# Kernel tuning notes

Measured on AMD Instinct MI355X. Metric: run time of the kernel, lower is better.

## Reference

```python
import jax, jax.numpy as jnp
import numpy as np

HIDDEN = 1024
SENT = 1024
NS = 8192
NK = 8192


def setup_inputs() -> dict:
    key = jax.random.key(0)
    ks = jax.random.split(key, 6)
    scale = 0.02
    return {
        "sentences_embedding": jax.random.normal(ks[0], (NS, SENT), dtype=jnp.float32),
        "knowledge_embedding": jax.random.normal(ks[1], (NK, 2 * HIDDEN), dtype=jnp.float32),
        "Ws": jax.random.normal(ks[2], (HIDDEN, SENT), dtype=jnp.float32) * scale,
        "bs": jnp.zeros((HIDDEN,), dtype=jnp.float32),
        "Wk": jax.random.normal(ks[3], (HIDDEN, 2 * HIDDEN), dtype=jnp.float32) * scale,
        "bk": jnp.zeros((HIDDEN,), dtype=jnp.float32),
    }


def reference(sentences_embedding, knowledge_embedding, Ws, bs, Wk, bk):
    # S: [Ns, hidden], K: [Nk, hidden] (torch Linear: x @ W.T + b)
    S = sentences_embedding @ Ws.T + bs
    K = knowledge_embedding @ Wk.T + bk
    V = knowledge_embedding  # [Nk, 2*hidden]
    scores = S @ K.T  # [Ns, Nk]
    # NOTE: softmax over dim=0 (across sentences), per the original module
    attns = jax.nn.softmax(scores, axis=0)
    fused_knowledge = attns @ V  # [Ns, 2*hidden]
    return (attns, fused_knowledge)
```

## Files before the change

### kernel.cpp

```cpp
#include <hip/hip_runtime.h>
#include <hip/hip_bf16.h>
#include <math.h>

typedef __bf16 bf16_t;
typedef __bf16 bf16x8 __attribute__((ext_vector_type(8)));
typedef __bf16 bf16x4v __attribute__((ext_vector_type(4)));
typedef float floatx4 __attribute__((ext_vector_type(4)));

#define BM 128
#define BN 128
#define BK 64
#define LDT 72

__device__ __forceinline__ void gload_lds16(const void* g, void* l) {
    __builtin_amdgcn_global_load_lds(
        (__attribute__((address_space(1))) void*)g,
        (__attribute__((address_space(3))) void*)l,
        16, 0, 0);
}

__device__ __forceinline__ void split8(const float* p, bf16x8& hi, bf16x8& lo) {
    const float4* q = (const float4*)p;
    float4 a = q[0], b = q[1];
    float v[8] = { a.x, a.y, a.z, a.w, b.x, b.y, b.z, b.w };
#pragma unroll
    for (int i = 0; i < 8; ++i) {
        bf16_t h = (bf16_t)v[i];
        hi[i] = h;
        lo[i] = (bf16_t)(v[i] - (float)h);
    }
}

__device__ __forceinline__ bf16x8 ld8cvt(const float* p) {
    const float4* q = (const float4*)p;
    float4 a = q[0], b = q[1];
    bf16x8 r;
    r[0] = (bf16_t)a.x; r[1] = (bf16_t)a.y; r[2] = (bf16_t)a.z; r[3] = (bf16_t)a.w;
    r[4] = (bf16_t)b.x; r[5] = (bf16_t)b.y; r[6] = (bf16_t)b.z; r[7] = (bf16_t)b.w;
    return r;
}

template<bool OUT_SPLIT, bool HAS_BIAS>
__global__ __launch_bounds__(256, 2)
void gemm_nt_split(const float* __restrict__ A, const float* __restrict__ B,
                   const float* __restrict__ bias,
                   void* __restrict__ C0, bf16_t* __restrict__ Clo,
                   int M, int N, int K)
{
    __shared__ bf16_t Ah[BM * LDT];
    __shared__ bf16_t Al[BM * LDT];
    __shared__ bf16_t Bh[BN * LDT];
    __shared__ bf16_t Bl[BN * LDT];

    const int t    = threadIdx.x;
    const int m0   = blockIdx.x * BM;
    const int n0   = blockIdx.y * BN;
    const int lane = t & 63;
    const int wm   = ((t >> 6) & 1) * 64;
    const int wn   = (t >> 7) * 64;
    const int lr   = lane & 15;
    const int lg   = lane >> 4;

    floatx4 acc[4][4] = {};

    for (int k0 = 0; k0 < K; k0 += BK) {
#pragma unroll
        for (int i = 0; i < 4; ++i) {
            int idx = t + i * 256;
            int row = idx >> 3;
            int col = (idx & 7) << 3;
            bf16x8 h, l;
            split8(&A[(size_t)(m0 + row) * K + k0 + col], h, l);
            *(bf16x8*)&Ah[row * LDT + col] = h;
            *(bf16x8*)&Al[row * LDT + col] = l;
            split8(&B[(size_t)(n0 + row) * K + k0 + col], h, l);
            *(bf16x8*)&Bh[row * LDT + col] = h;
            *(bf16x8*)&Bl[row * LDT + col] = l;
        }
        __syncthreads();
#pragma unroll
        for (int ks = 0; ks < BK; ks += 32) {
            bf16x8 ah[4], al[4], bh[4], bl[4];
#pragma unroll
            for (int mi = 0; mi < 4; ++mi) {
                ah[mi] = *(const bf16x8*)&Ah[(wm + mi * 16 + lr) * LDT + ks + lg * 8];
                al[mi] = *(const bf16x8*)&Al[(wm + mi * 16 + lr) * LDT + ks + lg * 8];
            }
#pragma unroll
            for (int ni = 0; ni < 4; ++ni) {
                bh[ni] = *(const bf16x8*)&Bh[(wn + ni * 16 + lr) * LDT + ks + lg * 8];
                bl[ni] = *(const bf16x8*)&Bl[(wn + ni * 16 + lr) * LDT + ks + lg * 8];
            }
#pragma unroll
            for (int mi = 0; mi < 4; ++mi)
#pragma unroll
                for (int ni = 0; ni < 4; ++ni) {
                    acc[mi][ni] = __builtin_amdgcn_mfma_f32_16x16x32_bf16(ah[mi], bh[ni], acc[mi][ni], 0, 0, 0);
                    acc[mi][ni] = __builtin_amdgcn_mfma_f32_16x16x32_bf16(ah[mi], bl[ni], acc[mi][ni], 0, 0, 0);
                    acc[mi][ni] = __builtin_amdgcn_mfma_f32_16x16x32_bf16(al[mi], bh[ni], acc[mi][ni], 0, 0, 0);
                }
        }
        __syncthreads();
    }

#pragma unroll
    for (int mi = 0; mi < 4; ++mi)
#pragma unroll
        for (int ni = 0; ni < 4; ++ni) {
            int col = n0 + wn + ni * 16 + lr;
            float bv = 0.0f;
            if constexpr (HAS_BIAS) bv = bias[col];
#pragma unroll
            for (int r = 0; r < 4; ++r) {
                int row = m0 + wm + mi * 16 + lg * 4 + r;
                float v = acc[mi][ni][r] + bv;
                if constexpr (OUT_SPLIT) {
                    bf16_t h = (bf16_t)v;
                    ((bf16_t*)C0)[(size_t)row * N + col] = h;
                    Clo[(size_t)row * N + col] = (bf16_t)(v - (float)h);
                } else {
                    ((float*)C0)[(size_t)row * N + col] = v;
                }
            }
        }
}

__global__ __launch_bounds__(256, 2)
void gemm_nt_pre_async(const bf16_t* __restrict__ Ahi, const bf16_t* __restrict__ Alo,
                       const bf16_t* __restrict__ Bhi, const bf16_t* __restrict__ Blo,
                       float* __restrict__ C, float* __restrict__ pm,
                       float* __restrict__ pz, int M, int N, int K)
{
    __shared__ bf16_t Ah[BM * BK];
    __shared__ bf16_t Al[BM * BK];
    __shared__ bf16_t Bh[BN * BK];
    __shared__ bf16_t Bl[BN * BK];
    __shared__ float red_m[2][128];
    __shared__ float red_z[2][128];

    const int t    = threadIdx.x;
    const int m0   = blockIdx.x * BM;
    const int n0   = blockIdx.y * BN;
    const int lane = t & 63;
    const int wv   = t >> 6;
    const int widm = (t >> 6) & 1;
    const int wm   = widm * 64;
    const int wn   = (t >> 7) * 64;
    const int lr   = lane & 15;
    const int lg   = lane >> 4;
    const int lrow = lane >> 3;
    const int lcol = (((lane & 7) ^ lrow) * 8);
    const int swz  = (lr & 7) << 3;

    floatx4 acc[4][4] = {};

    for (int k0 = 0; k0 < K; k0 += BK) {
#pragma unroll
        for (int i = 0; i < 4; ++i) {
            const int seg = wv * 4 + i;
            const int row = seg * 8 + lrow;
            const size_t ga = (size_t)(m0 + row) * K + k0 + lcol;
            const size_t gb = (size_t)(n0 + row) * K + k0 + lcol;
            gload_lds16(&Ahi[ga], &Ah[seg * 512]);
            gload_lds16(&Alo[ga], &Al[seg * 512]);
            gload_lds16(&Bhi[gb], &Bh[seg * 512]);
            gload_lds16(&Blo[gb], &Bl[seg * 512]);
        }
        __syncthreads();
#pragma unroll
        for (int ks = 0; ks < BK; ks += 32) {
            const int cA = (ks + lg * 8) ^ swz;
            bf16x8 ah[4], al[4], bh[4], bl[4];
#pragma unroll
            for (int mi = 0; mi < 4; ++mi) {
                ah[mi] = *(const bf16x8*)&Ah[(wm + mi * 16 + lr) * BK + cA];
                al[mi] = *(const bf16x8*)&Al[(wm + mi * 16 + lr) * BK + cA];
            }
#pragma unroll
            for (int ni = 0; ni < 4; ++ni) {
                bh[ni] = *(const bf16x8*)&Bh[(wn + ni * 16 + lr) * BK + cA];
                bl[ni] = *(const bf16x8*)&Bl[(wn + ni * 16 + lr) * BK + cA];
            }
#pragma unroll
            for (int mi = 0; mi < 4; ++mi)
#pragma unroll
                for (int ni = 0; ni < 4; ++ni) {
                    acc[mi][ni] = __builtin_amdgcn_mfma_f32_16x16x32_bf16(ah[mi], bh[ni], acc[mi][ni], 0, 0, 0);
                    acc[mi][ni] = __builtin_amdgcn_mfma_f32_16x16x32_bf16(ah[mi], bl[ni], acc[mi][ni], 0, 0, 0);
                    acc[mi][ni] = __builtin_amdgcn_mfma_f32_16x16x32_bf16(al[mi], bh[ni], acc[mi][ni], 0, 0, 0);
                }
        }
        __syncthreads();
    }

#pragma unroll
    for (int mi = 0; mi < 4; ++mi)
#pragma unroll
        for (int ni = 0; ni < 4; ++ni) {
            int col = n0 + wn + ni * 16 + lr;
#pragma unroll
            for (int r = 0; r < 4; ++r) {
                int row = m0 + wm + mi * 16 + lg * 4 + r;
                C[(size_t)row * N + col] = acc[mi][ni][r];
            }
        }

#pragma unroll
    for (int ni = 0; ni < 4; ++ni) {
        float lm = -INFINITY;
#pragma unroll
        for (int mi = 0; mi < 4; ++mi)
#pragma unroll
            for (int r = 0; r < 4; ++r) lm = fmaxf(lm, acc[mi][ni][r]);
        float lz = 0.0f;
#pragma unroll
        for (int mi = 0; mi < 4; ++mi)
#pragma unroll
            for (int r = 0; r < 4; ++r) lz += __expf(acc[mi][ni][r] - lm);
#pragma unroll
        for (int off = 16; off <= 32; off <<= 1) {
            float om = __shfl_xor(lm, off);
            float oz = __shfl_xor(lz, off);
            float nm = fmaxf(lm, om);
            lz = lz * __expf(lm - nm) + oz * __expf(om - nm);
            lm = nm;
        }
        if (lg == 0) {
            red_m[widm][wn + ni * 16 + lr] = lm;
            red_z[widm][wn + ni * 16 + lr] = lz;
        }
    }
    __syncthreads();
    if (t < 128) {
        float a = red_m[0][t], b = red_m[1][t];
        float za = red_z[0][t], zb = red_z[1][t];
        float mb = fmaxf(a, b);
        float z  = za * __expf(a - mb) + zb * __expf(b - mb);
        pm[(size_t)blockIdx.x * 8192 + n0 + t] = mb;
        pz[(size_t)blockIdx.x * 8192 + n0 + t] = z;
    }
}

__global__ __launch_bounds__(256, 2)
void gemm_nt_bf16_async(const bf16_t* __restrict__ A, const bf16_t* __restrict__ B,
                        float* __restrict__ C, int M, int N, int K)
{
    __shared__ bf16_t As[BM * BK];
    __shared__ bf16_t Bs[BN * BK];

    const int t    = threadIdx.x;
    const int m0   = blockIdx.x * BM;
    const int n0   = blockIdx.y * BN;
    const int lane = t & 63;
    const int wv   = t >> 6;
    const int wm   = ((t >> 6) & 1) * 64;
    const int wn   = (t >> 7) * 64;
    const int lr   = lane & 15;
    const int lg   = lane >> 4;
    const int lrow = lane >> 3;
    const int lcol = (((lane & 7) ^ lrow) * 8);
    const int swz  = (lr & 7) << 3;

    floatx4 acc[4][4] = {};

    for (int k0 = 0; k0 < K; k0 += BK) {
#pragma unroll
        for (int i = 0; i < 4; ++i) {
            const int seg = wv * 4 + i;
            const int row = seg * 8 + lrow;
            gload_lds16(&A[(size_t)(m0 + row) * K + k0 + lcol], &As[seg * 512]);
            gload_lds16(&B[(size_t)(n0 + row) * K + k0 + lcol], &Bs[seg * 512]);
        }
        __syncthreads();
#pragma unroll
        for (int ks = 0; ks < BK; ks += 32) {
            const int cA = (ks + lg * 8) ^ swz;
            bf16x8 a[4], b[4];
#pragma unroll
            for (int mi = 0; mi < 4; ++mi)
                a[mi] = *(const bf16x8*)&As[(wm + mi * 16 + lr) * BK + cA];
#pragma unroll
            for (int ni = 0; ni < 4; ++ni)
                b[ni] = *(const bf16x8*)&Bs[(wn + ni * 16 + lr) * BK + cA];
#pragma unroll
            for (int mi = 0; mi < 4; ++mi)
#pragma unroll
                for (int ni = 0; ni < 4; ++ni)
                    acc[mi][ni] = __builtin_amdgcn_mfma_f32_16x16x32_bf16(
                        a[mi], b[ni], acc[mi][ni], 0, 0, 0);
        }
        __syncthreads();
    }

#pragma unroll
    for (int mi = 0; mi < 4; ++mi)
#pragma unroll
        for (int ni = 0; ni < 4; ++ni) {
            int col = n0 + wn + ni * 16 + lr;
#pragma unroll
            for (int r = 0; r < 4; ++r) {
                int row = m0 + wm + mi * 16 + lg * 4 + r;
                C[(size_t)row * N + col] = acc[mi][ni][r];
            }
        }
}

__global__ __launch_bounds__(256)
void transpose_to_bf16(const float* __restrict__ src, bf16_t* __restrict__ dst,
                       int R, int Ccols)
{
    __shared__ float tile[64][65];
    const int r0 = blockIdx.x * 64;
    const int c0 = blockIdx.y * 64;
    const int tr = threadIdx.x >> 4;
    const int tc = (threadIdx.x & 15) * 4;
#pragma unroll
    for (int i = 0; i < 4; ++i) {
        int r = tr + i * 16;
        float4 v = *(const float4*)&src[(size_t)(r0 + r) * Ccols + c0 + tc];
        tile[r][tc + 0] = v.x; tile[r][tc + 1] = v.y;
        tile[r][tc + 2] = v.z; tile[r][tc + 3] = v.w;
    }
    __syncthreads();
#pragma unroll
    for (int i = 0; i < 4; ++i) {
        int c = tr + i * 16;
        bf16x4v o = { (bf16_t)tile[tc + 0][c], (bf16_t)tile[tc + 1][c],
                      (bf16_t)tile[tc + 2][c], (bf16_t)tile[tc + 3][c] };
        *(bf16x4v*)&dst[(size_t)(c0 + c) * R + r0 + tc] = o;
    }
}

__global__ __launch_bounds__(256)
void col_softmax_combine64(const float* __restrict__ pm, const float* __restrict__ pz,
                           float* __restrict__ mf, float* __restrict__ iz)
{
    int j = blockIdx.x * 256 + threadIdx.x;
    float m = -INFINITY;
#pragma unroll
    for (int c = 0; c < 64; ++c) m = fmaxf(m, pm[(size_t)c * 8192 + j]);
    float z = 0.0f;
#pragma unroll
    for (int c = 0; c < 64; ++c) z += pz[(size_t)c * 8192 + j] * __expf(pm[(size_t)c * 8192 + j] - m);
    mf[j] = m;
    iz[j] = 1.0f / z;
}

__global__ __launch_bounds__(256)
void normalize_attn(float* __restrict__ sc, const float* __restrict__ mf,
                    const float* __restrict__ iz)
{
    size_t base = ((size_t)blockIdx.x * 256 + threadIdx.x) * 4;
    int j = (int)(base & 8191);
    float4 s  = *(float4*)&sc[base];
    float4 m4 = *(const float4*)&mf[j];
    float4 z4 = *(const float4*)&iz[j];
    s.x = __expf(s.x - m4.x) * z4.x;
    s.y = __expf(s.y - m4.y) * z4.y;
    s.z = __expf(s.z - m4.z) * z4.z;
    s.w = __expf(s.w - m4.w) * z4.w;
    *(float4*)&sc[base] = s;
}

__global__ __launch_bounds__(256)
void normalize_attn_bf16(float* __restrict__ sc, const float* __restrict__ mf,
                         const float* __restrict__ iz, bf16_t* __restrict__ ab)
{
    size_t base = ((size_t)blockIdx.x * 256 + threadIdx.x) * 4;
    int j = (int)(base & 8191);
    float4 s  = *(float4*)&sc[base];
    float4 m4 = *(const float4*)&mf[j];
    float4 z4 = *(const float4*)&iz[j];
    s.x = __expf(s.x - m4.x) * z4.x;
    s.y = __expf(s.y - m4.y) * z4.y;
    s.z = __expf(s.z - m4.z) * z4.z;
    s.w = __expf(s.w - m4.w) * z4.w;
    *(float4*)&sc[base] = s;
    bf16x4v b = { (bf16_t)s.x, (bf16_t)s.y, (bf16_t)s.z, (bf16_t)s.w };
    *(bf16x4v*)&ab[base] = b;
}

extern "C" void kernel_launch(void* const* d_in, const int* in_sizes, int n_in,
                              void* d_out, int out_size, void* d_ws, size_t ws_size,
                              hipStream_t stream) {
    const float* sent  = (const float*)d_in[0];
    const float* knowl = (const float*)d_in[1];
    const float* Ws    = (const float*)d_in[2];
    const float* bs    = (const float*)d_in[3];
    const float* Wk    = (const float*)d_in[4];
    const float* bk    = (const float*)d_in[5];

    float* attns = (float*)d_out;
    float* fused = (float*)d_out + (size_t)8192 * 8192;

    const size_t MB = 1024 * 1024;
    char* ws = (char*)d_ws;
    bf16_t* Shi = (bf16_t*)(ws + 0 * MB);
    bf16_t* Slo = (bf16_t*)(ws + 16 * MB);
    bf16_t* Khi = (bf16_t*)(ws + 32 * MB);
    bf16_t* Klo = (bf16_t*)(ws + 48 * MB);

    dim3 blk(256);
    gemm_nt_split<true, true><<<dim3(64, 8), blk, 0, stream>>>(
        sent, Ws, bs, Shi, Slo, 8192, 1024, 1024);
    gemm_nt_split<true, true><<<dim3(64, 8), blk, 0, stream>>>(
        knowl, Wk, bk, Khi, Klo, 8192, 1024, 2048);

    const size_t NEED = 166 * MB;
    if (ws_size >= NEED) {
        bf16_t* Ab = (bf16_t*)(ws);
        bf16_t* Vt = (bf16_t*)(ws + 128 * MB);
        float*  pm = (float*)(ws + 160 * MB);
        float*  pz = (float*)(ws + 162 * MB);
        float*  mf = (float*)(ws + 164 * MB);
        float*  iz = mf + 8192;

        transpose_to_bf16<<<dim3(128, 32), blk, 0, stream>>>(knowl, Vt, 8192, 2048);
        gemm_nt_pre_async<<<dim3(64, 64), blk, 0, stream>>>(
            Shi, Slo, Khi, Klo, attns, pm, pz, 8192, 8192, 1024);
        col_softmax_combine64<<<dim3(32), blk, 0, stream>>>(pm, pz, mf, iz);
        normalize_attn_bf16<<<dim3(65536), blk, 0, stream>>>(attns, mf, iz, Ab);
        gemm_nt_bf16_async<<<dim3(64, 16), blk, 0, stream>>>(
            Ab, Vt, fused, 8192, 2048, 8192);
    } else {
        float* pm = (float*)(ws + 64 * MB);
        float* pz = (float*)(ws + 66 * MB);
        float* mf = (float*)(ws + 68 * MB);
        float* iz = mf + 8192;

        gemm_nt_pre_async<<<dim3(64, 64), blk, 0, stream>>>(
            Shi, Slo, Khi, Klo, attns, pm, pz, 8192, 8192, 1024);
        col_softmax_combine64<<<dim3(32), blk, 0, stream>>>(pm, pz, mf, iz);
        bf16_t* Ab = (bf16_t*)(ws);
        normalize_attn_bf16<<<dim3(65536), blk, 0, stream>>>(attns, mf, iz, Ab);
        bf16_t* Vt = (bf16_t*)(ws + 128 * MB);
        transpose_to_bf16<<<dim3(128, 32), blk, 0, stream>>>(knowl, Vt, 8192, 2048);
        gemm_nt_bf16_async<<<dim3(64, 16), blk, 0, stream>>>(
            Ab, Vt, fused, 8192, 2048, 8192);
    }
}
```

Baseline: 1.286 ms.

## Pre-split fp32 projection inputs into bf16 hi/lo and use async-LDS projection GEMM

Adds a split_pair kernel that converts the sentence, knowledge and weight matrices into bf16 hi/lo pairs up front, and a new projection GEMM that streams these pre-split operands straight into LDS with global_load_lds. The split conversion is no longer redone inside each projection tile. It also reorders the fallback path and moves the V transpose after the scores GEMM. The cost is extra full passes over the inputs and a larger workspace requirement (172MB), with the old path kept as a fallback.

```diff
diff --git a/kernel.cpp b/kernel.cpp
--- a/kernel.cpp
+++ b/kernel.cpp
@@ -31,13 +31,15 @@
     }
 }
 
-__device__ __forceinline__ bf16x8 ld8cvt(const float* p) {
-    const float4* q = (const float4*)p;
-    float4 a = q[0], b = q[1];
-    bf16x8 r;
-    r[0] = (bf16_t)a.x; r[1] = (bf16_t)a.y; r[2] = (bf16_t)a.z; r[3] = (bf16_t)a.w;
-    r[4] = (bf16_t)b.x; r[5] = (bf16_t)b.y; r[6] = (bf16_t)b.z; r[7] = (bf16_t)b.w;
-    return r;
+__global__ __launch_bounds__(256)
+void split_pair(const float* __restrict__ x, bf16_t* __restrict__ hi,
+                bf16_t* __restrict__ lo)
+{
+    size_t i = ((size_t)blockIdx.x * 256 + threadIdx.x) * 8;
+    bf16x8 h, l;
+    split8(&x[i], h, l);
+    *(bf16x8*)&hi[i] = h;
+    *(bf16x8*)&lo[i] = l;
 }
 
 template<bool OUT_SPLIT, bool HAS_BIAS>
@@ -121,6 +123,89 @@
                 } else {
                     ((float*)C0)[(size_t)row * N + col] = v;
                 }
+            }
+        }
+}
+
+__global__ __launch_bounds__(256, 2)
+void gemm_nt_pre_split_out(const bf16_t* __restrict__ Ahi, const bf16_t* __restrict__ Alo,
+                           const bf16_t* __restrict__ Bhi, const bf16_t* __restrict__ Blo,
+                           const float* __restrict__ bias,
+                           bf16_t* __restrict__ Chi, bf16_t* __restrict__ Clo,
+                           int M, int N, int K)
+{
+    __shared__ bf16_t Ah[BM * BK];
+    __shared__ bf16_t Al[BM * BK];
+    __shared__ bf16_t Bh[BN * BK];
+    __shared__ bf16_t Bl[BN * BK];
+
+    const int t    = threadIdx.x;
+    const int m0   = blockIdx.x * BM;
+    const int n0   = blockIdx.y * BN;
+    const int lane = t & 63;
+    const int wv   = t >> 6;
+    const int wm   = ((t >> 6) & 1) * 64;
+    const int wn   = (t >> 7) * 64;
+    const int lr   = lane & 15;
+    const int lg   = lane >> 4;
+    const int lrow = lane >> 3;
+    const int lcol = (((lane & 7) ^ lrow) * 8);
+    const int swz  = (lr & 7) << 3;
+
+    floatx4 acc[4][4] = {};
+
+    for (int k0 = 0; k0 < K; k0 += BK) {
+#pragma unroll
+        for (int i = 0; i < 4; ++i) {
+            const int seg = wv * 4 + i;
+            const int row = seg * 8 + lrow;
+            const size_t ga = (size_t)(m0 + row) * K + k0 + lcol;
+            const size_t gb = (size_t)(n0 + row) * K + k0 + lcol;
+            gload_lds16(&Ahi[ga], &Ah[seg * 512]);
+            gload_lds16(&Alo[ga], &Al[seg * 512]);
+            gload_lds16(&Bhi[gb], &Bh[seg * 512]);
+            gload_lds16(&Blo[gb], &Bl[seg * 512]);
+        }
+        __syncthreads();
+#pragma unroll
+        for (int ks = 0; ks < BK; ks += 32) {
+            const int cA = (ks + lg * 8) ^ swz;
+            bf16x8 ah[4], al[4], bh[4], bl[4];
+#pragma unroll
+            for (int mi = 0; mi < 4; ++mi) {
+                ah[mi] = *(const bf16x8*)&Ah[(wm + mi * 16 + lr) * BK + cA];
+                al[mi] = *(const bf16x8*)&Al[(wm + mi * 16 + lr) * BK + cA];
+            }
+#pragma unroll
+            for (int ni = 0; ni < 4; ++ni) {
+                bh[ni] = *(const bf16x8*)&Bh[(wn + ni * 16 + lr) * BK + cA];
+                bl[ni] = *(const bf16x8*)&Bl[(wn + ni * 16 + lr) * BK + cA];
+            }
+#pragma unroll
+            for (int mi = 0; mi < 4; ++mi)
+#pragma unroll
+                for (int ni = 0; ni < 4; ++ni) {
+                    acc[mi][ni] = __builtin_amdgcn_mfma_f32_16x16x32_bf16(ah[mi], bh[ni], acc[mi][ni], 0, 0, 0);
+                    acc[mi][ni] = __builtin_amdgcn_mfma_f32_16x16x32_bf16(ah[mi], bl[ni], acc[mi][ni], 0, 0, 0);
+                    acc[mi][ni] = __builtin_amdgcn_mfma_f32_16x16x32_bf16(al[mi], bh[ni], acc[mi][ni], 0, 0, 0);
+                }
+        }
+        __syncthreads();
+    }
+
+#pragma unroll
+    for (int mi = 0; mi < 4; ++mi)
+#pragma unroll
+        for (int ni = 0; ni < 4; ++ni) {
+            int col = n0 + wn + ni * 16 + lr;
+            float bv = bias[col];
+#pragma unroll
+            for (int r = 0; r < 4; ++r) {
+                int row = m0 + wm + mi * 16 + lg * 4 + r;
+                float v = acc[mi][ni][r] + bv;
+                bf16_t h = (bf16_t)v;
+                Chi[(size_t)row * N + col] = h;
+                Clo[(size_t)row * N + col] = (bf16_t)(v - (float)h);
             }
         }
 }
@@ -347,22 +432,6 @@
 }
 
 __global__ __launch_bounds__(256)
-void normalize_attn(float* __restrict__ sc, const float* __restrict__ mf,
-                    const float* __restrict__ iz)
-{
-    size_t base = ((size_t)blockIdx.x * 256 + threadIdx.x) * 4;
-    int j = (int)(base & 8191);
-    float4 s  = *(float4*)&sc[base];
-    float4 m4 = *(const float4*)&mf[j];
-    float4 z4 = *(const float4*)&iz[j];
-    s.x = __expf(s.x - m4.x) * z4.x;
-    s.y = __expf(s.y - m4.y) * z4.y;
-    s.z = __expf(s.z - m4.z) * z4.z;
-    s.w = __expf(s.w - m4.w) * z4.w;
-    *(float4*)&sc[base] = s;
-}
-
-__global__ __launch_bounds__(256)
 void normalize_attn_bf16(float* __restrict__ sc, const float* __restrict__ mf,
                          const float* __restrict__ iz, bf16_t* __restrict__ ab)
 {
@@ -395,46 +464,65 @@
 
     const size_t MB = 1024 * 1024;
     char* ws = (char*)d_ws;
-    bf16_t* Shi = (bf16_t*)(ws + 0 * MB);
-    bf16_t* Slo = (bf16_t*)(ws + 16 * MB);
-    bf16_t* Khi = (bf16_t*)(ws + 32 * MB);
-    bf16_t* Klo = (bf16_t*)(ws + 48 * MB);
-
     dim3 blk(256);
-    gemm_nt_split<true, true><<<dim3(64, 8), blk, 0, stream>>>(
-        sent, Ws, bs, Shi, Slo, 8192, 1024, 1024);
-    gemm_nt_split<true, true><<<dim3(64, 8), blk, 0, stream>>>(
-        knowl, Wk, bk, Khi, Klo, 8192, 1024, 2048);
-
-    const size_t NEED = 166 * MB;
-    if (ws_size >= NEED) {
-        bf16_t* Ab = (bf16_t*)(ws);
-        bf16_t* Vt = (bf16_t*)(ws + 128 * MB);
-        float*  pm = (float*)(ws + 160 * MB);
-        float*  pz = (float*)(ws + 162 * MB);
-        float*  mf = (float*)(ws + 164 * MB);
-        float*  iz = mf + 8192;
-
-        transpose_to_bf16<<<dim3(128, 32), blk, 0, stream>>>(knowl, Vt, 8192, 2048);
+
+    const size_t NEED_FAST = 172 * MB;
+    if (ws_size >= NEED_FAST) {
+        bf16_t* SEhi = (bf16_t*)(ws + 0 * MB);
+        bf16_t* SElo = (bf16_t*)(ws + 16 * MB);
+        bf16_t* KNhi = (bf16_t*)(ws + 32 * MB);
+        bf16_t* KNlo = (bf16_t*)(ws + 64 * MB);
+        bf16_t* Shi  = (bf16_t*)(ws + 96 * MB);
+        bf16_t* Slo  = (bf16_t*)(ws + 112 * MB);
+        bf16_t* Khi  = (bf16_t*)(ws + 128 * MB);
+        bf16_t* Klo  = (bf16_t*)(ws + 144 * MB);
+        bf16_t* Wshi = (bf16_t*)(ws + 160 * MB);
+        bf16_t* Wslo = (bf16_t*)(ws + 162 * MB);
+        bf16_t* Wkhi = (bf16_t*)(ws + 164 * MB);
+        bf16_t* Wklo = (bf16_t*)(ws + 168 * MB);
+        bf16_t* Ab   = (bf16_t*)(ws + 0 * MB);
+        bf16_t* Vt   = (bf16_t*)(ws + 128 * MB);
+        float*  pm   = (float*)(ws + 160 * MB);
+        float*  pz   = (float*)(ws + 162 * MB);
+        float*  mf   = (float*)(ws + 164 * MB);
+        float*  iz   = mf + 8192;
+
+        split_pair<<<dim3(4096), blk, 0, stream>>>(sent,  SEhi, SElo);
+        split_pair<<<dim3(8192), blk, 0, stream>>>(knowl, KNhi, KNlo);
+        split_pair<<<dim3(512),  blk, 0, stream>>>(Ws,    Wshi, Wslo);
+        split_pair<<<dim3(1024), blk, 0, stream>>>(Wk,    Wkhi, Wklo);
+        gemm_nt_pre_split_out<<<dim3(64, 8), blk, 0, stream>>>(
+            SEhi, SElo, Wshi, Wslo, bs, Shi, Slo, 8192, 1024, 1024);
+        gemm_nt_pre_split_out<<<dim3(64, 8), blk, 0, stream>>>(
+            KNhi, KNlo, Wkhi, Wklo, bk, Khi, Klo, 8192, 1024, 2048);
         gemm_nt_pre_async<<<dim3(64, 64), blk, 0, stream>>>(
             Shi, Slo, Khi, Klo, attns, pm, pz, 8192, 8192, 1024);
+        transpose_to_bf16<<<dim3(128, 32), blk, 0, stream>>>(knowl, Vt, 8192, 2048);
         col_softmax_combine64<<<dim3(32), blk, 0, stream>>>(pm, pz, mf, iz);
         normalize_attn_bf16<<<dim3(65536), blk, 0, stream>>>(attns, mf, iz, Ab);
         gemm_nt_bf16_async<<<dim3(64, 16), blk, 0, stream>>>(
             Ab, Vt, fused, 8192, 2048, 8192);
     } else {
-        float* pm = (float*)(ws + 64 * MB);
-        float* pz = (float*)(ws + 66 * MB);
-        float* mf = (float*)(ws + 68 * MB);
-        float* iz = mf + 8192;
-
+        bf16_t* Shi = (bf16_t*)(ws + 0 * MB);
+        bf16_t* Slo = (bf16_t*)(ws + 16 * MB);
+        bf16_t* Khi = (bf16_t*)(ws + 32 * MB);
+        bf16_t* Klo = (bf16_t*)(ws + 48 * MB);
+        bf16_t* Ab  = (bf16_t*)(ws);
+        bf16_t* Vt  = (bf16_t*)(ws + 128 * MB);
+        float*  pm  = (float*)(ws + 160 * MB);
+        float*  pz  = (float*)(ws + 162 * MB);
+        float*  mf  = (float*)(ws + 164 * MB);
+        float*  iz  = mf + 8192;
+
+        gemm_nt_split<true, true><<<dim3(64, 8), blk, 0, stream>>>(
+            sent, Ws, bs, Shi, Slo, 8192, 1024, 1024);
+        gemm_nt_split<true, true><<<dim3(64, 8), blk, 0, stream>>>(
+            knowl, Wk, bk, Khi, Klo, 8192, 1024, 2048);
         gemm_nt_pre_async<<<dim3(64, 64), blk, 0, stream>>>(
             Shi, Slo, Khi, Klo, attns, pm, pz, 8192, 8192, 1024);
+        transpose_to_bf16<<<dim3(128, 32), blk, 0, stream>>>(knowl, Vt, 8192, 2048);
         col_softmax_combine64<<<dim3(32), blk, 0, stream>>>(pm, pz, mf, iz);
-        bf16_t* Ab = (bf16_t*)(ws);
         normalize_attn_bf16<<<dim3(65536), blk, 0, stream>>>(attns, mf, iz, Ab);
-        bf16_t* Vt = (bf16_t*)(ws + 128 * MB);
-        transpose_to_bf16<<<dim3(128, 32), blk, 0, stream>>>(knowl, Vt, 8192, 2048);
         gemm_nt_bf16_async<<<dim3(64, 16), blk, 0, stream>>>(
             Ab, Vt, fused, 8192, 2048, 8192);
     }
```

Result: slower. 1.319 ms (+2.5%).
